# Optimization experiments

Measured on AMD Instinct MI355X. Metric: run time of the kernel, lower is better.

Reference implementation:

```python
import jax, jax.numpy as jnp
import numpy as np

N = 100000      # nodes
E = 1600000     # edges (avg degree 16)
F_IN = 128
HID = 128
C = 64
EPS = 1e-5      # BatchNorm1d default eps


def setup_inputs() -> dict:
    key = jax.random.key(0)
    ks = jax.random.split(key, 10)
    return {
        "features": jax.random.normal(ks[0], (N, F_IN), dtype=jnp.float32),
        "edge_src": jax.random.randint(ks[1], (E,), 0, N, dtype=jnp.int32),
        "edge_dst": jax.random.randint(ks[2], (E,), 0, N, dtype=jnp.int32),
        "edge_weight": jax.random.uniform(ks[3], (E,), dtype=jnp.float32),
        "W1": jax.random.normal(ks[4], (F_IN, HID), dtype=jnp.float32) / np.sqrt(F_IN),
        "b1": jnp.zeros((HID,), dtype=jnp.float32),
        "gamma1": jnp.ones((HID,), dtype=jnp.float32),
        "beta1": jnp.zeros((HID,), dtype=jnp.float32),
        "mean1": jnp.zeros((HID,), dtype=jnp.float32),
        "var1": jnp.ones((HID,), dtype=jnp.float32),
        "W2": jax.random.normal(ks[5], (HID, C), dtype=jnp.float32) / np.sqrt(HID),
        "b2": jnp.zeros((C,), dtype=jnp.float32),
        "embedding_prev": jax.random.normal(ks[6], (N, C), dtype=jnp.float32),
        "sensitive_mask": jax.random.bernoulli(ks[7], 0.2, (N,)),
        "insensitive_mask": jax.random.bernoulli(ks[8], 0.5, (N,)),
    }


def reference(features, edge_src, edge_dst, edge_weight, W1, b1, gamma1, beta1,
              mean1, var1, W2, b2, embedding_prev, sensitive_mask, insensitive_mask):
    # GCNConv: h = A_hat @ (X W) + b, with A_hat given as (edge_src, edge_dst, edge_weight)
    def gcn_conv(x, W, b):
        xw = x @ W                                        # [N, d_out]
        msg = xw[edge_src] * edge_weight[:, None]         # [E, d_out] gather + scale
        return jax.ops.segment_sum(msg, edge_dst, num_segments=N) + b

    h = gcn_conv(features, W1, b1)
    # BatchNorm1d (eval mode: running stats), then ReLU (dropout is a no-op in eval)
    h = gamma1 * (h - mean1) * jax.lax.rsqrt(var1 + EPS) + beta1
    h = jax.nn.relu(h)
    h = gcn_conv(h, W2, b2)

    # combine_embedding (delta merge):
    # 1) rows NOT in v_sensitive are replaced by the previous embedding
    # 2) rows in v_insensitive get the freshly-computed feature ADDED (gathered pre-replacement)
    keep = ~sensitive_mask                                # complement set, as in the source
    out = jnp.where(keep[:, None], embedding_prev, h)
    out = out + jnp.where(insensitive_mask[:, None], h, jnp.float32(0.0))

    return jax.nn.log_softmax(out, axis=-1), out
```

## Files before the change

### kernel.cpp

```cpp
#include <hip/hip_runtime.h>
#include <math.h>

#define F_IN 128
#define HID  128
#define CDIM 64
#define BN_EPS 1e-5f
#define SCAN_CHUNK 1024

typedef unsigned int u32;
typedef unsigned short u16;
typedef __attribute__((ext_vector_type(8))) short bf16x8;
typedef __attribute__((ext_vector_type(4))) float f32x4;

__device__ __forceinline__ float bf_lo(u32 p) {
    u32 x = p << 16; return __builtin_bit_cast(float, x);
}
__device__ __forceinline__ float bf_hi(u32 p) {
    u32 x = p & 0xffff0000u; return __builtin_bit_cast(float, x);
}
__device__ __forceinline__ u16 f2bf(float f) {
    u32 x = __builtin_bit_cast(u32, f);
    return (u16)((x + 0x7fffu + ((x >> 16) & 1u)) >> 16);
}
__device__ __forceinline__ u32 pack2(float a, float b) {
    return (u32)f2bf(a) | ((u32)f2bf(b) << 16);
}

__device__ __forceinline__ bf16x8 frag_ld(const u16* lds, int row, int kb) {
    return *(const bf16x8*)&lds[row * 128 + (kb ^ ((row & 7) << 3))];
}

__global__ __launch_bounds__(256) void wt_prep(const float* __restrict__ W1,
                                               const float* __restrict__ W2,
                                               u16* __restrict__ wt1,
                                               u16* __restrict__ wt2) {
    int t = blockIdx.x * 256 + threadIdx.x;
    if (t < 128 * 128) {
        int k = t >> 7, c = t & 127;
        wt1[c * 128 + (k ^ ((c & 7) << 3))] = f2bf(W1[t]);
    } else if (t < 128 * 128 + 128 * 64) {
        int t2 = t - 128 * 128;
        int k = t2 >> 6, c = t2 & 63;
        wt2[c * 128 + (k ^ ((c & 7) << 3))] = f2bf(W2[t2]);
    }
}

__global__ __launch_bounds__(256) void gemm_xw1_mfma(const float* __restrict__ X,
                                                     const u16* __restrict__ wt1,
                                                     u32* __restrict__ Yb, int N) {
    __shared__ u16 wl[128 * 128];
    __shared__ u16 xl[64 * 128];
    for (int i = threadIdx.x; i < 2048; i += 256)
        ((uint4*)wl)[i] = ((const uint4*)wt1)[i];
    const int l  = threadIdx.x & 63;
    const int wv = threadIdx.x >> 6;
    const int r16 = wv * 16;
    const int lr = l & 15;
    const int kq = l >> 4;
    const int ntiles = (N + 63) >> 6;
    for (int tile = blockIdx.x; tile < ntiles; tile += gridDim.x) {
        const int row0 = tile << 6;
        __syncthreads();
        for (int i = threadIdx.x; i < 2048; i += 256) {
            int r = i >> 5, c4 = i & 31;
            int gr = row0 + r;
            float4 v = make_float4(0.f, 0.f, 0.f, 0.f);
            if (gr < N) v = *(const float4*)&X[(size_t)gr * F_IN + c4 * 4];
            uint2 p;
            p.x = pack2(v.x, v.y);
            p.y = pack2(v.z, v.w);
            *(uint2*)&xl[r * 128 + ((c4 * 4) ^ ((r & 7) << 3))] = p;
        }
        __syncthreads();
        f32x4 acc[8];
        #pragma unroll
        for (int c = 0; c < 8; ++c) acc[c] = (f32x4){0.f, 0.f, 0.f, 0.f};
        #pragma unroll
        for (int k0 = 0; k0 < 128; k0 += 32) {
            int kb = k0 + kq * 8;
            bf16x8 xf = frag_ld(xl, r16 + lr, kb);
            #pragma unroll
            for (int c = 0; c < 8; ++c) {
                bf16x8 wf = frag_ld(wl, c * 16 + lr, kb);
                acc[c] = __builtin_amdgcn_mfma_f32_16x16x32_bf16(wf, xf, acc[c], 0, 0, 0);
            }
        }
        int grow = row0 + r16 + lr;
        if (grow < N) {
            #pragma unroll
            for (int c = 0; c < 8; ++c) {
                uint2 o;
                o.x = pack2(acc[c][0], acc[c][1]);
                o.y = pack2(acc[c][2], acc[c][3]);
                *(uint2*)&Yb[(size_t)grow * 64 + c * 8 + kq * 2] = o;
            }
        }
    }
}

__global__ __launch_bounds__(256) void gemm_xw2_mfma(const u32* __restrict__ Hb,
                                                     const u16* __restrict__ wt2,
                                                     u32* __restrict__ Yb, int N) {
    __shared__ u16 wl[64 * 128];
    __shared__ u16 xl[64 * 128];
    for (int i = threadIdx.x; i < 1024; i += 256)
        ((uint4*)wl)[i] = ((const uint4*)wt2)[i];
    const int l  = threadIdx.x & 63;
    const int wv = threadIdx.x >> 6;
    const int r16 = wv * 16;
    const int lr = l & 15;
    const int kq = l >> 4;
    const int ntiles = (N + 63) >> 6;
    for (int tile = blockIdx.x; tile < ntiles; tile += gridDim.x) {
        const int row0 = tile << 6;
        __syncthreads();
        for (int i = threadIdx.x; i < 1024; i += 256) {
            int r = i >> 4, c8 = i & 15;
            int gr = row0 + r;
            uint4 v = make_uint4(0u, 0u, 0u, 0u);
            if (gr < N) v = *(const uint4*)&Hb[(size_t)gr * 64 + c8 * 4];
            *(uint4*)&xl[r * 128 + ((c8 * 8) ^ ((r & 7) << 3))] = v;
        }
        __syncthreads();
        f32x4 acc[4];
        #pragma unroll
        for (int c = 0; c < 4; ++c) acc[c] = (f32x4){0.f, 0.f, 0.f, 0.f};
        #pragma unroll
        for (int k0 = 0; k0 < 128; k0 += 32) {
            int kb = k0 + kq * 8;
            bf16x8 xf = frag_ld(xl, r16 + lr, kb);
            #pragma unroll
            for (int c = 0; c < 4; ++c) {
                bf16x8 wf = frag_ld(wl, c * 16 + lr, kb);
                acc[c] = __builtin_amdgcn_mfma_f32_16x16x32_bf16(wf, xf, acc[c], 0, 0, 0);
            }
        }
        int grow = row0 + r16 + lr;
        if (grow < N) {
            #pragma unroll
            for (int c = 0; c < 4; ++c) {
                uint2 o;
                o.x = pack2(acc[c][0], acc[c][1]);
                o.y = pack2(acc[c][2], acc[c][3]);
                *(uint2*)&Yb[(size_t)grow * 32 + c * 8 + kq * 2] = o;
            }
        }
    }
}

__global__ __launch_bounds__(256) void hist_kernel(const int* __restrict__ dst,
                                                   int* __restrict__ counts, int E) {
    int gid = blockIdx.x * 256 + threadIdx.x;
    int stride = gridDim.x * 256;
    for (; gid < E; gid += stride)
        atomicAdd(&counts[__builtin_nontemporal_load(&dst[gid])], 1);
}

__global__ __launch_bounds__(256) void scan_sums(const int* __restrict__ counts,
                                                 int* __restrict__ bsums, int N) {
    __shared__ int sdata[256];
    int base = blockIdx.x * SCAN_CHUNK + threadIdx.x * 4;
    int t = 0;
    #pragma unroll
    for (int j = 0; j < 4; ++j) { int i = base + j; if (i < N) t += counts[i]; }
    sdata[threadIdx.x] = t; __syncthreads();
    for (int off = 128; off > 0; off >>= 1) {
        if (threadIdx.x < off) sdata[threadIdx.x] += sdata[threadIdx.x + off];
        __syncthreads();
    }
    if (threadIdx.x == 0) bsums[blockIdx.x] = sdata[0];
}

__global__ void scan_offsets(const int* __restrict__ bsums, int* __restrict__ boffs,
                             int nb, int* __restrict__ row_ptr, int N, int E) {
    if (threadIdx.x == 0 && blockIdx.x == 0) {
        int run = 0;
        for (int i = 0; i < nb; ++i) { boffs[i] = run; run += bsums[i]; }
        row_ptr[N] = E;
    }
}

__global__ __launch_bounds__(256) void scan_write(const int* __restrict__ counts,
                                                  const int* __restrict__ boffs,
                                                  int* __restrict__ row_ptr,
                                                  int* __restrict__ cursor, int N) {
    __shared__ int sdata[256];
    int base = blockIdx.x * SCAN_CHUNK + threadIdx.x * 4;
    int v[4]; int tsum = 0;
    #pragma unroll
    for (int j = 0; j < 4; ++j) {
        int i = base + j;
        v[j] = (i < N) ? counts[i] : 0;
        tsum += v[j];
    }
    sdata[threadIdx.x] = tsum; __syncthreads();
    for (int off = 1; off < 256; off <<= 1) {
        int t = (threadIdx.x >= off) ? sdata[threadIdx.x - off] : 0;
        __syncthreads();
        sdata[threadIdx.x] += t;
        __syncthreads();
    }
    int off0 = sdata[threadIdx.x] - tsum + boffs[blockIdx.x];
    #pragma unroll
    for (int j = 0; j < 4; ++j) {
        int i = base + j;
        if (i < N) { row_ptr[i] = off0; cursor[i] = off0; off0 += v[j]; }
    }
}

__global__ __launch_bounds__(256) void fill_kernel(const int* __restrict__ src,
                                                   const int* __restrict__ dst,
                                                   const float* __restrict__ w,
                                                   int* __restrict__ cursor,
                                                   uint2* __restrict__ es_packed,
                                                   int E, int N) {
    const int slice = blockIdx.x & 7;
    const int sw = (N + 7) >> 3;
    const int lo = slice * sw;
    const int hi = (lo + sw < N) ? (lo + sw) : N;
    int gid = (blockIdx.x >> 3) * 256 + threadIdx.x;
    const int stride = (gridDim.x >> 3) * 256;
    for (; gid < E; gid += stride) {
        int d = __builtin_nontemporal_load(&dst[gid]);
        if (d >= lo && d < hi) {
            int pos = atomicAdd(&cursor[d], 1);
            uint2 pk;
            pk.x = (u32)__builtin_nontemporal_load(&src[gid]);
            pk.y = __builtin_bit_cast(u32, __builtin_nontemporal_load(&w[gid]));
            es_packed[pos] = pk;
        }
    }
}

__global__ void bn_prep(const float* __restrict__ b1, const float* __restrict__ gamma,
                        const float* __restrict__ beta, const float* __restrict__ mean,
                        const float* __restrict__ var, float* __restrict__ scale,
                        float* __restrict__ shift) {
    int f = threadIdx.x;
    if (f < HID) {
        float sc = gamma[f] * rsqrtf(var[f] + BN_EPS);
        scale[f] = sc;
        shift[f] = beta[f] + sc * (b1[f] - mean[f]);
    }
}

__global__ __launch_bounds__(256) void gather1_kernel(
        const u32* __restrict__ XWb, const int* __restrict__ row_ptr,
        const uint2* __restrict__ es, const float* __restrict__ scale,
        const float* __restrict__ shift, u32* __restrict__ Hb, int N) {
    int r = blockIdx.x * 4 + (threadIdx.x >> 6);
    if (r >= N) return;
    int f = threadIdx.x & 63;
    int q = f >> 4;
    int fc = f & 15;
    int beg = row_ptr[r], end = row_ptr[r + 1];
    float acc[8];
    #pragma unroll
    for (int j = 0; j < 8; ++j) acc[j] = 0.f;
    for (int base = beg; base < end; base += 64) {
        int m = end - base; if (m > 64) m = 64;
        uint2 pk = (f < m) ? es[base + f] : make_uint2(0u, 0u);
        int   se = (int)pk.x;
        float we = __builtin_bit_cast(float, pk.y);
        for (int k = 0; k < m; k += 4) {
            int k0 = k + q;
            int   sk = __shfl(se, k0, 64);
            float wk = __shfl(we, k0, 64);
            uint4 x = *(const uint4*)&XWb[(size_t)sk * 64 + 4 * fc];
            acc[0] = fmaf(bf_lo(x.x), wk, acc[0]);
            acc[1] = fmaf(bf_hi(x.x), wk, acc[1]);
            acc[2] = fmaf(bf_lo(x.y), wk, acc[2]);
            acc[3] = fmaf(bf_hi(x.y), wk, acc[3]);
            acc[4] = fmaf(bf_lo(x.z), wk, acc[4]);
            acc[5] = fmaf(bf_hi(x.z), wk, acc[5]);
            acc[6] = fmaf(bf_lo(x.w), wk, acc[6]);
            acc[7] = fmaf(bf_hi(x.w), wk, acc[7]);
        }
    }
    #pragma unroll
    for (int j = 0; j < 8; ++j) {
        acc[j] += __shfl_xor(acc[j], 16, 64);
        acc[j] += __shfl_xor(acc[j], 32, 64);
    }
    if (q == 0) {
        float4 sc0 = *(const float4*)&scale[8 * fc];
        float4 sc1 = *(const float4*)&scale[8 * fc + 4];
        float4 sh0 = *(const float4*)&shift[8 * fc];
        float4 sh1 = *(const float4*)&shift[8 * fc + 4];
        float h0 = fmaf(acc[0], sc0.x, sh0.x);
        float h1 = fmaf(acc[1], sc0.y, sh0.y);
        float h2 = fmaf(acc[2], sc0.z, sh0.z);
        float h3 = fmaf(acc[3], sc0.w, sh0.w);
        float h4 = fmaf(acc[4], sc1.x, sh1.x);
        float h5 = fmaf(acc[5], sc1.y, sh1.y);
        float h6 = fmaf(acc[6], sc1.z, sh1.z);
        float h7 = fmaf(acc[7], sc1.w, sh1.w);
        uint4 o;
        o.x = pack2(h0 > 0.f ? h0 : 0.f, h1 > 0.f ? h1 : 0.f);
        o.y = pack2(h2 > 0.f ? h2 : 0.f, h3 > 0.f ? h3 : 0.f);
        o.z = pack2(h4 > 0.f ? h4 : 0.f, h5 > 0.f ? h5 : 0.f);
        o.w = pack2(h6 > 0.f ? h6 : 0.f, h7 > 0.f ? h7 : 0.f);
        *(uint4*)&Hb[(size_t)r * 64 + 4 * fc] = o;
    }
}

__global__ __launch_bounds__(256) void gather2_final(
        const u32* __restrict__ XW2b, const int* __restrict__ row_ptr,
        const uint2* __restrict__ es, const float* __restrict__ b2,
        const float* __restrict__ prev, const int* __restrict__ sens,
        const int* __restrict__ ins, float* __restrict__ out_lsm,
        float* __restrict__ out_emb, int N) {
    int r = blockIdx.x * 4 + (threadIdx.x >> 6);
    if (r >= N) return;
    int f = threadIdx.x & 63;
    int q = f >> 4;
    int fc = f & 15;
    int beg = row_ptr[r], end = row_ptr[r + 1];
    float a0 = 0.f, a1 = 0.f, a2 = 0.f, a3 = 0.f;
    for (int base = beg; base < end; base += 64) {
        int m = end - base; if (m > 64) m = 64;
        uint2 pk = (f < m) ? es[base + f] : make_uint2(0u, 0u);
        int   se = (int)pk.x;
        float we = __builtin_bit_cast(float, pk.y);
        for (int k = 0; k < m; k += 4) {
            int k0 = k + q;
            int   sk = __shfl(se, k0, 64);
            float wk = __shfl(we, k0, 64);
            uint2 x = *(const uint2*)&XW2b[(size_t)sk * 32 + 2 * fc];
            a0 = fmaf(bf_lo(x.x), wk, a0);
            a1 = fmaf(bf_hi(x.x), wk, a1);
            a2 = fmaf(bf_lo(x.y), wk, a2);
            a3 = fmaf(bf_hi(x.y), wk, a3);
        }
    }
    a0 += __shfl_xor(a0, 16, 64); a0 += __shfl_xor(a0, 32, 64);
    a1 += __shfl_xor(a1, 16, 64); a1 += __shfl_xor(a1, 32, 64);
    a2 += __shfl_xor(a2, 16, 64); a2 += __shfl_xor(a2, 32, 64);
    a3 += __shfl_xor(a3, 16, 64); a3 += __shfl_xor(a3, 32, 64);

    float4 bb = *(const float4*)&b2[4 * fc];
    float h0 = a0 + bb.x, h1 = a1 + bb.y, h2 = a2 + bb.z, h3 = a3 + bb.w;
    bool s_ = sens[r] != 0;
    bool i_ = ins[r] != 0;
    float4 pv = *(const float4*)&prev[(size_t)r * CDIM + 4 * fc];
    float o0 = (s_ ? h0 : pv.x) + (i_ ? h0 : 0.f);
    float o1 = (s_ ? h1 : pv.y) + (i_ ? h1 : 0.f);
    float o2 = (s_ ? h2 : pv.z) + (i_ ? h2 : 0.f);
    float o3 = (s_ ? h3 : pv.w) + (i_ ? h3 : 0.f);
    float mm = fmaxf(fmaxf(o0, o1), fmaxf(o2, o3));
    #pragma unroll
    for (int off = 8; off > 0; off >>= 1) mm = fmaxf(mm, __shfl_xor(mm, off, 64));
    float s = expf(o0 - mm) + expf(o1 - mm) + expf(o2 - mm) + expf(o3 - mm);
    #pragma unroll
    for (int off = 8; off > 0; off >>= 1) s += __shfl_xor(s, off, 64);
    float lse = mm + logf(s);
    if (q == 0) {
        *(float4*)&out_lsm[(size_t)r * CDIM + 4 * fc] =
            make_float4(o0 - lse, o1 - lse, o2 - lse, o3 - lse);
        *(float4*)&out_emb[(size_t)r * CDIM + 4 * fc] =
            make_float4(o0, o1, o2, o3);
    }
}

extern "C" void kernel_launch(void* const* d_in, const int* in_sizes, int n_in,
                              void* d_out, int out_size, void* d_ws, size_t ws_size,
                              hipStream_t stream) {
    const float* features = (const float*)d_in[0];
    const int*   esrc     = (const int*)d_in[1];
    const int*   edst     = (const int*)d_in[2];
    const float* ew       = (const float*)d_in[3];
    const float* W1       = (const float*)d_in[4];
    const float* b1       = (const float*)d_in[5];
    const float* gamma1   = (const float*)d_in[6];
    const float* beta1    = (const float*)d_in[7];
    const float* mean1    = (const float*)d_in[8];
    const float* var1     = (const float*)d_in[9];
    const float* W2       = (const float*)d_in[10];
    const float* b2       = (const float*)d_in[11];
    const float* prev     = (const float*)d_in[12];
    const int*   sens     = (const int*)d_in[13];
    const int*   ins      = (const int*)d_in[14];

    const int N = in_sizes[0] / F_IN;
    const int E = in_sizes[1];
    const int nb = (N + SCAN_CHUNK - 1) / SCAN_CHUNK;

    u16* wt1   = (u16*)d_ws;
    u16* wt2   = wt1 + 128 * 128;
    u32* xw1b  = (u32*)d_ws + 12288;
    u32* hb    = xw1b + (size_t)N * 64;
    u32* xw2b  = hb + (size_t)N * 64;
    uint2* es_packed = (uint2*)(xw2b + (size_t)N * 32);
    float* scale = (float*)(es_packed + E);
    float* shift = scale + HID;
    int* row_ptr = (int*)(shift + HID);
    int* cursor  = row_ptr + (N + 1);
    int* bsums   = cursor + N;
    int* boffs   = bsums + nb;

    float* out_lsm = (float*)d_out;
    float* out_emb = out_lsm + (size_t)N * CDIM;

    wt_prep<<<96, 256, 0, stream>>>(W1, W2, wt1, wt2);

    hipMemsetAsync(cursor, 0, (size_t)N * sizeof(int), stream);
    hist_kernel<<<(E + 255) / 256, 256, 0, stream>>>(edst, cursor, E);
    scan_sums<<<nb, 256, 0, stream>>>(cursor, bsums, N);
    scan_offsets<<<1, 64, 0, stream>>>(bsums, boffs, nb, row_ptr, N, E);
    scan_write<<<nb, 256, 0, stream>>>(cursor, boffs, row_ptr, cursor, N);
    fill_kernel<<<2048, 256, 0, stream>>>(esrc, edst, ew, cursor,
                                          es_packed, E, N);
    bn_prep<<<1, 128, 0, stream>>>(b1, gamma1, beta1, mean1, var1, scale, shift);

    const int nt64 = (N + 63) / 64;
    gemm_xw1_mfma<<<nt64, 256, 0, stream>>>(features, wt1, xw1b, N);
    gather1_kernel<<<(N + 3) / 4, 256, 0, stream>>>(xw1b, row_ptr, es_packed,
                                                    scale, shift, hb, N);
    gemm_xw2_mfma<<<nt64, 256, 0, stream>>>(hb, wt2, xw2b, N);
    gather2_final<<<(N + 3) / 4, 256, 0, stream>>>(xw2b, row_ptr, es_packed,
                                                   b2, prev, sens, ins,
                                                   out_lsm, out_emb, N);
}
```

Baseline: 463.5 us.

## Record per-edge rank in histogram pass to make CSR fill atomic-free

The histogram kernel now stores the atomicAdd return value as a 16-bit per-edge rank within its destination. The fill kernel computes each edge's slot as row_ptr[dst] plus that rank, so it needs no atomics and no longer scans all edges eight times across destination slices. This removes a second round of atomics and the repeated reads of dst, at the cost of writing and reading an extra 2-byte rank array. It assumes in-degree stays below 65536.

```diff
diff --git a/kernel.cpp b/kernel.cpp
--- a/kernel.cpp
+++ b/kernel.cpp
@@ -9,6 +9,7 @@
 
 typedef unsigned int u32;
 typedef unsigned short u16;
+typedef unsigned long long u64;
 typedef __attribute__((ext_vector_type(8))) short bf16x8;
 typedef __attribute__((ext_vector_type(4))) float f32x4;
 
@@ -149,11 +150,15 @@
 }
 
 __global__ __launch_bounds__(256) void hist_kernel(const int* __restrict__ dst,
-                                                   int* __restrict__ counts, int E) {
+                                                   int* __restrict__ counts,
+                                                   u16* __restrict__ rank, int E) {
     int gid = blockIdx.x * 256 + threadIdx.x;
     int stride = gridDim.x * 256;
-    for (; gid < E; gid += stride)
-        atomicAdd(&counts[__builtin_nontemporal_load(&dst[gid])], 1);
+    for (; gid < E; gid += stride) {
+        int d = __builtin_nontemporal_load(&dst[gid]);
+        int r = atomicAdd(&counts[d], 1);
+        __builtin_nontemporal_store((u16)r, &rank[gid]);
+    }
 }
 
 __global__ __launch_bounds__(256) void scan_sums(const int* __restrict__ counts,
@@ -182,8 +187,7 @@
 
 __global__ __launch_bounds__(256) void scan_write(const int* __restrict__ counts,
                                                   const int* __restrict__ boffs,
-                                                  int* __restrict__ row_ptr,
-                                                  int* __restrict__ cursor, int N) {
+                                                  int* __restrict__ row_ptr, int N) {
     __shared__ int sdata[256];
     int base = blockIdx.x * SCAN_CHUNK + threadIdx.x * 4;
     int v[4]; int tsum = 0;
@@ -204,31 +208,25 @@
     #pragma unroll
     for (int j = 0; j < 4; ++j) {
         int i = base + j;
-        if (i < N) { row_ptr[i] = off0; cursor[i] = off0; off0 += v[j]; }
+        if (i < N) { row_ptr[i] = off0; off0 += v[j]; }
     }
 }
 
 __global__ __launch_bounds__(256) void fill_kernel(const int* __restrict__ src,
                                                    const int* __restrict__ dst,
                                                    const float* __restrict__ w,
-                                                   int* __restrict__ cursor,
-                                                   uint2* __restrict__ es_packed,
-                                                   int E, int N) {
-    const int slice = blockIdx.x & 7;
-    const int sw = (N + 7) >> 3;
-    const int lo = slice * sw;
-    const int hi = (lo + sw < N) ? (lo + sw) : N;
-    int gid = (blockIdx.x >> 3) * 256 + threadIdx.x;
-    const int stride = (gridDim.x >> 3) * 256;
+                                                   const u16* __restrict__ rank,
+                                                   const int* __restrict__ row_ptr,
+                                                   u64* __restrict__ es_packed,
+                                                   int E) {
+    int gid = blockIdx.x * 256 + threadIdx.x;
+    int stride = gridDim.x * 256;
     for (; gid < E; gid += stride) {
         int d = __builtin_nontemporal_load(&dst[gid]);
-        if (d >= lo && d < hi) {
-            int pos = atomicAdd(&cursor[d], 1);
-            uint2 pk;
-            pk.x = (u32)__builtin_nontemporal_load(&src[gid]);
-            pk.y = __builtin_bit_cast(u32, __builtin_nontemporal_load(&w[gid]));
-            es_packed[pos] = pk;
-        }
+        int pos = row_ptr[d] + (int)__builtin_nontemporal_load(&rank[gid]);
+        u64 lo = (u32)__builtin_nontemporal_load(&src[gid]);
+        u64 hi = (u64)__builtin_bit_cast(u32, __builtin_nontemporal_load(&w[gid])) << 32;
+        __builtin_nontemporal_store(lo | hi, &es_packed[pos]);
     }
 }
 
@@ -390,34 +388,37 @@
     u32* xw1b  = (u32*)d_ws + 12288;
     u32* hb    = xw1b + (size_t)N * 64;
     u32* xw2b  = hb + (size_t)N * 64;
-    uint2* es_packed = (uint2*)(xw2b + (size_t)N * 32);
+    u64* es_packed = (u64*)(xw2b + (size_t)N * 32);
     float* scale = (float*)(es_packed + E);
     float* shift = scale + HID;
     int* row_ptr = (int*)(shift + HID);
-    int* cursor  = row_ptr + (N + 1);
-    int* bsums   = cursor + N;
+    int* counts  = row_ptr + (N + 1);
+    int* bsums   = counts + N;
     int* boffs   = bsums + nb;
+    u16* rank16  = (u16*)(boffs + nb);
 
     float* out_lsm = (float*)d_out;
     float* out_emb = out_lsm + (size_t)N * CDIM;
 
     wt_prep<<<96, 256, 0, stream>>>(W1, W2, wt1, wt2);
 
-    hipMemsetAsync(cursor, 0, (size_t)N * sizeof(int), stream);
-    hist_kernel<<<(E + 255) / 256, 256, 0, stream>>>(edst, cursor, E);
-    scan_sums<<<nb, 256, 0, stream>>>(cursor, bsums, N);
+    hipMemsetAsync(counts, 0, (size_t)N * sizeof(int), stream);
+    hist_kernel<<<(E + 255) / 256, 256, 0, stream>>>(edst, counts, rank16, E);
+    scan_sums<<<nb, 256, 0, stream>>>(counts, bsums, N);
     scan_offsets<<<1, 64, 0, stream>>>(bsums, boffs, nb, row_ptr, N, E);
-    scan_write<<<nb, 256, 0, stream>>>(cursor, boffs, row_ptr, cursor, N);
-    fill_kernel<<<2048, 256, 0, stream>>>(esrc, edst, ew, cursor,
-                                          es_packed, E, N);
+    scan_write<<<nb, 256, 0, stream>>>(counts, boffs, row_ptr, N);
+    fill_kernel<<<2048, 256, 0, stream>>>(esrc, edst, ew, rank16, row_ptr,
+                                          es_packed, E);
     bn_prep<<<1, 128, 0, stream>>>(b1, gamma1, beta1, mean1, var1, scale, shift);
 
     const int nt64 = (N + 63) / 64;
     gemm_xw1_mfma<<<nt64, 256, 0, stream>>>(features, wt1, xw1b, N);
-    gather1_kernel<<<(N + 3) / 4, 256, 0, stream>>>(xw1b, row_ptr, es_packed,
+    gather1_kernel<<<(N + 3) / 4, 256, 0, stream>>>(xw1b, row_ptr,
+                                                    (const uint2*)es_packed,
                                                     scale, shift, hb, N);
     gemm_xw2_mfma<<<nt64, 256, 0, stream>>>(hb, wt2, xw2b, N);
-    gather2_final<<<(N + 3) / 4, 256, 0, stream>>>(xw2b, row_ptr, es_packed,
+    gather2_final<<<(N + 3) / 4, 256, 0, stream>>>(xw2b, row_ptr,
+                                                   (const uint2*)es_packed,
                                                    b2, prev, sens, ins,
                                                    out_lsm, out_emb, N);
 }
```

After: 442.1 us. -4.6%, faster.
